# Performance work log

Hardware: AMD Instinct MI355X
Metric: run time of the kernel (lower is better)

The kernel has to match this reference:

```python
import jax, jax.numpy as jnp
import numpy as np

EPS = 1e-7  # tf.keras.backend.epsilon()


def squash(v, axis=-1):
    s = jnp.sum(jnp.square(v), axis=axis, keepdims=True)
    scale = s / (1.0 + s) / jnp.sqrt(s + EPS)
    return scale * v


def setup_inputs() -> dict:
    key = jax.random.key(0)
    k1, k2 = jax.random.split(key)
    B, I, D = 64, 2048, 16   # batch, input_num_capsule, input_dim_capsule
    J, K = 32, 16            # num_capsule, dim_capsule
    inputs = jax.random.normal(k1, (B, I, D), dtype=jnp.float32)
    # glorot_uniform-ish init for W: [in_caps, num_caps, in_dim, dim_caps]
    limit = np.sqrt(6.0 / (D + K)).astype(np.float32)
    W = jax.random.uniform(k2, (I, J, D, K), dtype=jnp.float32, minval=-limit, maxval=limit)
    return {"inputs": inputs, "W": W}


def reference(inputs, W, routings=3):
    # u_hat[b,i,j,:] = inputs[b,i,:] @ W[i,j,:,:]
    u_hat = jnp.einsum('bid,ijdk->bijk', inputs, W)  # [B, I, J, K]
    B, I, J, _ = u_hat.shape
    b = jnp.zeros((B, I, J, 1), dtype=u_hat.dtype)
    outputs = None
    for r in range(routings):
        c = jax.nn.softmax(b, axis=2)                              # [B, I, J, 1]
        outputs = squash(jnp.sum(c * u_hat, axis=1, keepdims=True))  # [B, 1, J, K]
        if r < routings - 1:
            b = b + jnp.sum(u_hat * outputs, axis=-1, keepdims=True)
    return jnp.squeeze(outputs, axis=1)  # [B, J, K]
```

## Files before the change

kernel.cpp:

```cpp
#include <hip/hip_runtime.h>
#include <hip/hip_bf16.h>


#define B_ 64
#define I_ 2048
#define D_ 16
#define J_ 32
#define K_ 16
#define JK 512

typedef __attribute__((ext_vector_type(8))) short short8;
typedef __attribute__((ext_vector_type(4))) float float4v;

__device__ __forceinline__ unsigned short f2bf(float f) {
    union { float f; unsigned int i; } v;
    v.f = f;
    const unsigned int x = v.i;
    return (unsigned short)((x + 0x7fffu + ((x >> 16) & 1u)) >> 16);
}

__device__ __forceinline__ void unpack8(const uint4 r, float* u) {
    union { unsigned int i; float f; } t;
    t.i = r.x << 16;         u[0] = t.f;
    t.i = r.x & 0xffff0000u; u[1] = t.f;
    t.i = r.y << 16;         u[2] = t.f;
    t.i = r.y & 0xffff0000u; u[3] = t.f;
    t.i = r.z << 16;         u[4] = t.f;
    t.i = r.z & 0xffff0000u; u[5] = t.f;
    t.i = r.w << 16;         u[6] = t.f;
    t.i = r.w & 0xffff0000u; u[7] = t.f;
}

template <int CTRL>
__device__ __forceinline__ float dpp_add(float x) {
    union { float f; int i; } a, b;
    a.f = x;
    b.i = __builtin_amdgcn_update_dpp(0, a.i, CTRL, 0xf, 0xf, false);
    return x + b.f;
}

__global__ __launch_bounds__(256)
void caps_produce(const float* __restrict__ x, const float* __restrict__ W,
                  unsigned short* __restrict__ uhat) {
    __shared__ unsigned short wlds[32 * 384];
    __shared__ unsigned short zbuf[8];
    const int i = blockIdx.x;
    const int tid = threadIdx.x;

    if (tid < 8) zbuf[tid] = 0;

    const int lane = tid & 63;
    const int wv = tid >> 6;
    const int quad = lane >> 4;
    const int l15 = lane & 15;
    const int b = wv * 16 + l15;

    union { uint4 u; short8 s; } bfrag;
    {
        const float* xp = x + ((size_t)b * I_ + i) * D_ + (quad & 1) * 8;
        const float4 x0 = reinterpret_cast<const float4*>(xp)[0];
        const float4 x1 = reinterpret_cast<const float4*>(xp)[1];
        bfrag.u.x = ((unsigned int)f2bf(x0.y) << 16) | f2bf(x0.x);
        bfrag.u.y = ((unsigned int)f2bf(x0.w) << 16) | f2bf(x0.z);
        bfrag.u.z = ((unsigned int)f2bf(x1.y) << 16) | f2bf(x1.x);
        bfrag.u.w = ((unsigned int)f2bf(x1.w) << 16) | f2bf(x1.z);
        if (quad >= 2) { bfrag.u.x = 0; bfrag.u.y = 0; bfrag.u.z = 0; bfrag.u.w = 0; }
    }

    {
        const float* wbase = W + (size_t)i * (J_ * D_ * K_);
        const int k = tid & 15;
#pragma unroll
        for (int half = 0; half < 2; ++half) {
            const int j = (tid >> 4) + half * 16;
            const float* p = wbase + j * (D_ * K_) + k;
            float vals[16];
#pragma unroll
            for (int d = 0; d < 16; ++d) vals[d] = p[d * K_];
            unsigned int pk[8];
#pragma unroll
            for (int q = 0; q < 8; ++q)
                pk[q] = ((unsigned int)f2bf(vals[2 * q + 1]) << 16) |
                        f2bf(vals[2 * q]);
            uint4* dst = reinterpret_cast<uint4*>(wlds + j * 384 + k * 24);
            uint4 w0; w0.x = pk[0]; w0.y = pk[1]; w0.z = pk[2]; w0.w = pk[3];
            uint4 w1; w1.x = pk[4]; w1.y = pk[5]; w1.z = pk[6]; w1.w = pk[7];
            dst[0] = w0; dst[1] = w1;
        }
    }
    __syncthreads();

    const unsigned short* aptr =
        (quad >= 2) ? zbuf : (wlds + l15 * 24 + (quad & 1) * 8);
    const int astride = (quad >= 2) ? 0 : 384;

    unsigned short* ub = uhat + ((size_t)i * B_ + b) * JK + quad * 4;

#pragma unroll
    for (int j = 0; j < 32; ++j) {
        union { uint4 u; short8 s; } af;
        af.u = *reinterpret_cast<const uint4*>(aptr + (size_t)j * astride);
        float4v acc = {0.f, 0.f, 0.f, 0.f};
        acc = __builtin_amdgcn_mfma_f32_16x16x32_bf16(af.s, bfrag.s, acc,
                                                      0, 0, 0);
        uint2 pk;
        pk.x = ((unsigned int)f2bf(acc[1]) << 16) | f2bf(acc[0]);
        pk.y = ((unsigned int)f2bf(acc[3]) << 16) | f2bf(acc[2]);
        *reinterpret_cast<uint2*>(ub + j * 16) = pk;
    }
}

__global__ __launch_bounds__(256)
void caps_sum0(const unsigned short* __restrict__ uhat,
               float* __restrict__ spart2) {
    __shared__ float part[4][512];
    const int bq = blockIdx.x;
    const int b = bq >> 5, q = bq & 31;
    const int lane = threadIdx.x & 63;
    const int w = threadIdx.x >> 6;

    const unsigned short* up =
        uhat + ((size_t)(q * 64 + w * 16) * B_ + b) * JK + lane * 8;
    const size_t istride = (size_t)B_ * JK;

    float acc[8];
#pragma unroll
    for (int k = 0; k < 8; ++k) acc[k] = 0.f;

    for (int ii = 0; ii < 16; ii += 4) {
        uint4 r[4];
#pragma unroll
        for (int s = 0; s < 4; ++s)
            r[s] = *reinterpret_cast<const uint4*>(up + (size_t)(ii + s) * istride);
#pragma unroll
        for (int s = 0; s < 4; ++s) {
            float u[8];
            unpack8(r[s], u);
#pragma unroll
            for (int k = 0; k < 8; ++k) acc[k] += u[k];
        }
    }

    float4 o0, o1;
    o0.x = acc[0]; o0.y = acc[1]; o0.z = acc[2]; o0.w = acc[3];
    o1.x = acc[4]; o1.y = acc[5]; o1.z = acc[6]; o1.w = acc[7];
    reinterpret_cast<float4*>(&part[w][lane * 8])[0] = o0;
    reinterpret_cast<float4*>(&part[w][lane * 8])[1] = o1;
    __syncthreads();

    const int t = threadIdx.x;
#pragma unroll
    for (int e = 0; e < 2; ++e) {
        const int jk = t * 2 + e;
        spart2[(size_t)bq * 512 + jk] =
            part[0][jk] + part[1][jk] + part[2][jk] + part[3][jk];
    }
}

__global__ __launch_bounds__(512)
void caps_squash0(const float* __restrict__ spart2, float* __restrict__ vsum) {
    const int bl = blockIdx.x;
    const int jk = threadIdx.x;
    float s = 0.f;
#pragma unroll
    for (int p = 0; p < 32; ++p)
        s += spart2[(size_t)(bl * 32 + p) * 512 + jk];
    s *= (1.f / 32.f);
    float q = s * s;
    q += __shfl_xor(q, 1, 64);
    q += __shfl_xor(q, 2, 64);
    q += __shfl_xor(q, 4, 64);
    q += __shfl_xor(q, 8, 64);
    const float scale = q / ((1.f + q) * sqrtf(q + 1e-7f));
    vsum[bl * JK + jk] = scale * s;
}

__global__ __launch_bounds__(128)
void caps_route1(const unsigned short* __restrict__ uhat,
                 const float* __restrict__ vsum, float* __restrict__ spart) {
    __shared__ float mrg[32][17];
    const int tid = threadIdx.x;
    const int lane = tid & 63;
    const int wv = tid >> 6;
    const int bl = blockIdx.x >> 6;
    const int chunk = blockIdx.x & 63;
    const int h = lane >> 5;
    const int j = lane & 31;

    float v[16];
    {
        const float4* vp =
            reinterpret_cast<const float4*>(vsum + bl * JK + j * 16);
        const float4 a0 = vp[0], a1 = vp[1], a2 = vp[2], a3 = vp[3];
        v[0] = a0.x; v[1] = a0.y; v[2] = a0.z; v[3] = a0.w;
        v[4] = a1.x; v[5] = a1.y; v[6] = a1.z; v[7] = a1.w;
        v[8] = a2.x; v[9] = a2.y; v[10] = a2.z; v[11] = a2.w;
        v[12] = a3.x; v[13] = a3.y; v[14] = a3.z; v[15] = a3.w;
    }

    float acc[16];
#pragma unroll
    for (int k = 0; k < 16; ++k) acc[k] = 0.f;

    const unsigned short* up =
        uhat + ((size_t)(chunk * 32 + wv * 16 + h) * B_ + bl) * JK + j * 16;
    const size_t istride2 = (size_t)2 * B_ * JK;

    uint4 c0 = reinterpret_cast<const uint4*>(up)[0];
    uint4 c1 = reinterpret_cast<const uint4*>(up)[1];

#pragma unroll 4
    for (int t = 0; t < 8; ++t) {
        uint4 n0, n1;
        if (t < 7) {
            const uint4* np =
                reinterpret_cast<const uint4*>(up + (size_t)(t + 1) * istride2);
            n0 = np[0];
            n1 = np[1];
        }
        float u[16];
        unpack8(c0, u);
        unpack8(c1, u + 8);
        float p = 0.f;
#pragma unroll
        for (int k = 0; k < 16; ++k) p += u[k] * v[k];
        const float e = __expf(p);
        float S = e;
        S = dpp_add<0x111>(S);
        S = dpp_add<0x112>(S);
        S = dpp_add<0x114>(S);
        S = dpp_add<0x118>(S);
        S = dpp_add<0x142>(S);
        union { float f; int i; } sv, lo, hi;
        sv.f = S;
        lo.i = __builtin_amdgcn_readlane(sv.i, 31);
        hi.i = __builtin_amdgcn_readlane(sv.i, 63);
        const float Ssel = (h == 0) ? lo.f : hi.f;
        const float c = e * __builtin_amdgcn_rcpf(Ssel);
#pragma unroll
        for (int k = 0; k < 16; ++k) acc[k] += c * u[k];
        c0 = n0;
        c1 = n1;
    }

#pragma unroll
    for (int k = 0; k < 16; ++k) acc[k] += __shfl_xor(acc[k], 32, 64);

    if (wv == 1 && h == 0) {
#pragma unroll
        for (int k = 0; k < 16; ++k) mrg[j][k] = acc[k];
    }
    __syncthreads();

    if (wv == 0 && h == 0) {
        float* sp = spart + ((size_t)chunk * B_ + bl) * JK + j * 16;
#pragma unroll
        for (int q = 0; q < 4; ++q) {
            float4 o;
            o.x = acc[q * 4 + 0] + mrg[j][q * 4 + 0];
            o.y = acc[q * 4 + 1] + mrg[j][q * 4 + 1];
            o.z = acc[q * 4 + 2] + mrg[j][q * 4 + 2];
            o.w = acc[q * 4 + 3] + mrg[j][q * 4 + 3];
            reinterpret_cast<float4*>(sp)[q] = o;
        }
    }
}

template <int MODE>
__global__ __launch_bounds__(512)
void caps_squash(const float* __restrict__ spart, float* __restrict__ vsum,
                 float* __restrict__ out) {
    const int bl = blockIdx.x;
    const int jk = threadIdx.x;
    float s = 0.f;
#pragma unroll 8
    for (int p = 0; p < 64; ++p)
        s += spart[((size_t)p * B_ + bl) * JK + jk];
    float q = s * s;
    q += __shfl_xor(q, 1, 64);
    q += __shfl_xor(q, 2, 64);
    q += __shfl_xor(q, 4, 64);
    q += __shfl_xor(q, 8, 64);
    const float scale = q / ((1.f + q) * sqrtf(q + 1e-7f));
    const float v = scale * s;
    if (MODE == 1) vsum[bl * JK + jk] += v;
    else           out[(size_t)bl * JK + jk] = v;
}

extern "C" void kernel_launch(void* const* d_in, const int* in_sizes, int n_in,
                              void* d_out, int out_size, void* d_ws,
                              size_t ws_size, hipStream_t stream) {
    const float* x = (const float*)d_in[0];
    const float* W = (const float*)d_in[1];
    float* out = (float*)d_out;

    char* ws = (char*)d_ws;
    unsigned short* uhat = (unsigned short*)ws;
    float* spart = (float*)(ws + (size_t)B_ * I_ * JK * 2);
    float* vsum = spart + (size_t)64 * B_ * JK;

    caps_produce<<<I_, 256, 0, stream>>>(x, W, uhat);

    caps_sum0<<<2048, 256, 0, stream>>>(uhat, spart);
    caps_squash0<<<B_, 512, 0, stream>>>(spart, vsum);

    caps_route1<<<4096, 128, 0, stream>>>(uhat, vsum, spart);
    caps_squash<1><<<B_, 512, 0, stream>>>(spart, vsum, out);

    caps_route1<<<4096, 128, 0, stream>>>(uhat, vsum, spart);
    caps_squash<2><<<B_, 512, 0, stream>>>(spart, vsum, out);
}
```

Baseline: 209.8 us.

## Recompute u_hat on the fly per routing pass instead of materializing it

Drops the materialized bf16 u_hat buffer and instead recomputes u_hat with MFMA in each routing pass, fusing the agreement dot product, softmax over capsules (via an LDS exchange between the two j-halves) and the weighted sum into one kernel. Each block handles eight input capsules with double-buffered W tiles in LDS and writes per-block partial sums that a squash kernel reduces. This removes the large u_hat write and the repeated re-reads of it, at the cost of re-reading W and x and repeating the matmul three times (twice per pass in routing mode). Only 256 blocks launch, which may underfill the GPU, and the squash reduction now walks 256 partials instead of 64.

New measurement: 229.9 us. 9.6% more time.

```diff
diff --git a/kernel.cpp b/kernel.cpp
--- a/kernel.cpp
+++ b/kernel.cpp
@@ -8,6 +8,8 @@
 #define J_ 32
 #define K_ 16
 #define JK 512
+#define NBLK 256
+#define GI 8
 
 typedef __attribute__((ext_vector_type(8))) short short8;
 typedef __attribute__((ext_vector_type(4))) float float4v;
@@ -19,61 +21,49 @@
     return (unsigned short)((x + 0x7fffu + ((x >> 16) & 1u)) >> 16);
 }
 
-__device__ __forceinline__ void unpack8(const uint4 r, float* u) {
-    union { unsigned int i; float f; } t;
-    t.i = r.x << 16;         u[0] = t.f;
-    t.i = r.x & 0xffff0000u; u[1] = t.f;
-    t.i = r.y << 16;         u[2] = t.f;
-    t.i = r.y & 0xffff0000u; u[3] = t.f;
-    t.i = r.z << 16;         u[4] = t.f;
-    t.i = r.z & 0xffff0000u; u[5] = t.f;
-    t.i = r.w << 16;         u[6] = t.f;
-    t.i = r.w & 0xffff0000u; u[7] = t.f;
-}
-
-template <int CTRL>
-__device__ __forceinline__ float dpp_add(float x) {
-    union { float f; int i; } a, b;
-    a.f = x;
-    b.i = __builtin_amdgcn_update_dpp(0, a.i, CTRL, 0xf, 0xf, false);
-    return x + b.f;
-}
-
-__global__ __launch_bounds__(256)
-void caps_produce(const float* __restrict__ x, const float* __restrict__ W,
-                  unsigned short* __restrict__ uhat) {
-    __shared__ unsigned short wlds[32 * 384];
+template <int MODE>
+__global__ __launch_bounds__(512)
+void caps_pass(const float* __restrict__ x, const float* __restrict__ W,
+               const float* __restrict__ vsum, float* __restrict__ part) {
+    __shared__ unsigned short wlds[2][32 * 384];
     __shared__ unsigned short zbuf[8];
-    const int i = blockIdx.x;
+    __shared__ float ebuf[2][4][2][16];
     const int tid = threadIdx.x;
+    const int lane = tid & 63;
+    const int wv = tid >> 6;
+    const int bt = wv & 3;
+    const int jh = wv >> 2;
+    const int quad = lane >> 4;
+    const int l15 = lane & 15;
+    const int b = bt * 16 + l15;
+    const int i0 = blockIdx.x * GI;
 
     if (tid < 8) zbuf[tid] = 0;
 
-    const int lane = tid & 63;
-    const int wv = tid >> 6;
-    const int quad = lane >> 4;
-    const int l15 = lane & 15;
-    const int b = wv * 16 + l15;
-
-    union { uint4 u; short8 s; } bfrag;
-    {
-        const float* xp = x + ((size_t)b * I_ + i) * D_ + (quad & 1) * 8;
-        const float4 x0 = reinterpret_cast<const float4*>(xp)[0];
-        const float4 x1 = reinterpret_cast<const float4*>(xp)[1];
-        bfrag.u.x = ((unsigned int)f2bf(x0.y) << 16) | f2bf(x0.x);
-        bfrag.u.y = ((unsigned int)f2bf(x0.w) << 16) | f2bf(x0.z);
-        bfrag.u.z = ((unsigned int)f2bf(x1.y) << 16) | f2bf(x1.x);
-        bfrag.u.w = ((unsigned int)f2bf(x1.w) << 16) | f2bf(x1.z);
-        if (quad >= 2) { bfrag.u.x = 0; bfrag.u.y = 0; bfrag.u.z = 0; bfrag.u.w = 0; }
+    float4 vv[16];
+    if (MODE == 1) {
+#pragma unroll
+        for (int jj = 0; jj < 16; ++jj)
+            vv[jj] = reinterpret_cast<const float4*>(
+                vsum + b * JK + (jh * 16 + jj) * 16 + quad * 4)[0];
     }
 
-    {
-        const float* wbase = W + (size_t)i * (J_ * D_ * K_);
-        const int k = tid & 15;
+    float4 acc2[16];
 #pragma unroll
-        for (int half = 0; half < 2; ++half) {
-            const int j = (tid >> 4) + half * 16;
-            const float* p = wbase + j * (D_ * K_) + k;
+    for (int jj = 0; jj < 16; ++jj) {
+        acc2[jj].x = 0.f; acc2[jj].y = 0.f;
+        acc2[jj].z = 0.f; acc2[jj].w = 0.f;
+    }
+
+    const int sk = tid & 15;
+    const int sj = tid >> 4;
+
+    for (int t = 0; t < GI; ++t) {
+        const int i = i0 + t;
+        const int par = t & 1;
+
+        {
+            const float* p = W + (size_t)i * (J_ * D_ * K_) + sj * (D_ * K_) + sk;
             float vals[16];
 #pragma unroll
             for (int d = 0; d < 16; ++d) vals[d] = p[d * K_];
@@ -82,200 +72,96 @@
             for (int q = 0; q < 8; ++q)
                 pk[q] = ((unsigned int)f2bf(vals[2 * q + 1]) << 16) |
                         f2bf(vals[2 * q]);
-            uint4* dst = reinterpret_cast<uint4*>(wlds + j * 384 + k * 24);
+            uint4* dst = reinterpret_cast<uint4*>(&wlds[par][sj * 384 + sk * 24]);
             uint4 w0; w0.x = pk[0]; w0.y = pk[1]; w0.z = pk[2]; w0.w = pk[3];
             uint4 w1; w1.x = pk[4]; w1.y = pk[5]; w1.z = pk[6]; w1.w = pk[7];
             dst[0] = w0; dst[1] = w1;
         }
-    }
-    __syncthreads();
 
-    const unsigned short* aptr =
-        (quad >= 2) ? zbuf : (wlds + l15 * 24 + (quad & 1) * 8);
-    const int astride = (quad >= 2) ? 0 : 384;
+        union { uint4 u; short8 s; } bfrag;
+        {
+            const float* xp = x + ((size_t)b * I_ + i) * D_ + (quad & 1) * 8;
+            const float4 x0 = reinterpret_cast<const float4*>(xp)[0];
+            const float4 x1 = reinterpret_cast<const float4*>(xp)[1];
+            bfrag.u.x = ((unsigned int)f2bf(x0.y) << 16) | f2bf(x0.x);
+            bfrag.u.y = ((unsigned int)f2bf(x0.w) << 16) | f2bf(x0.z);
+            bfrag.u.z = ((unsigned int)f2bf(x1.y) << 16) | f2bf(x1.x);
+            bfrag.u.w = ((unsigned int)f2bf(x1.w) << 16) | f2bf(x1.z);
+            if (quad >= 2) { bfrag.u.x = 0; bfrag.u.y = 0; bfrag.u.z = 0; bfrag.u.w = 0; }
+        }
+        __syncthreads();
 
-    unsigned short* ub = uhat + ((size_t)i * B_ + b) * JK + quad * 4;
+        const unsigned short* aptr =
+            (quad >= 2) ? zbuf : (&wlds[par][0] + l15 * 24 + (quad & 1) * 8);
+        const int astride = (quad >= 2) ? 0 : 384;
 
+        if (MODE == 0) {
 #pragma unroll
-    for (int j = 0; j < 32; ++j) {
-        union { uint4 u; short8 s; } af;
-        af.u = *reinterpret_cast<const uint4*>(aptr + (size_t)j * astride);
-        float4v acc = {0.f, 0.f, 0.f, 0.f};
-        acc = __builtin_amdgcn_mfma_f32_16x16x32_bf16(af.s, bfrag.s, acc,
-                                                      0, 0, 0);
-        uint2 pk;
-        pk.x = ((unsigned int)f2bf(acc[1]) << 16) | f2bf(acc[0]);
-        pk.y = ((unsigned int)f2bf(acc[3]) << 16) | f2bf(acc[2]);
-        *reinterpret_cast<uint2*>(ub + j * 16) = pk;
-    }
-}
-
-__global__ __launch_bounds__(256)
-void caps_sum0(const unsigned short* __restrict__ uhat,
-               float* __restrict__ spart2) {
-    __shared__ float part[4][512];
-    const int bq = blockIdx.x;
-    const int b = bq >> 5, q = bq & 31;
-    const int lane = threadIdx.x & 63;
-    const int w = threadIdx.x >> 6;
-
-    const unsigned short* up =
-        uhat + ((size_t)(q * 64 + w * 16) * B_ + b) * JK + lane * 8;
-    const size_t istride = (size_t)B_ * JK;
-
-    float acc[8];
+            for (int jj = 0; jj < 16; ++jj) {
+                const int j = jh * 16 + jj;
+                union { uint4 u; short8 s; } af;
+                af.u = *reinterpret_cast<const uint4*>(aptr + (size_t)j * astride);
+                float4v a = {0.f, 0.f, 0.f, 0.f};
+                a = __builtin_amdgcn_mfma_f32_16x16x32_bf16(af.s, bfrag.s, a,
+                                                            0, 0, 0);
+                acc2[jj].x += a[0]; acc2[jj].y += a[1];
+                acc2[jj].z += a[2]; acc2[jj].w += a[3];
+            }
+        } else {
+            float e[16];
+            float E = 0.f;
 #pragma unroll
-    for (int k = 0; k < 8; ++k) acc[k] = 0.f;
-
-    for (int ii = 0; ii < 16; ii += 4) {
-        uint4 r[4];
+            for (int jj = 0; jj < 16; ++jj) {
+                const int j = jh * 16 + jj;
+                union { uint4 u; short8 s; } af;
+                af.u = *reinterpret_cast<const uint4*>(aptr + (size_t)j * astride);
+                float4v a = {0.f, 0.f, 0.f, 0.f};
+                a = __builtin_amdgcn_mfma_f32_16x16x32_bf16(af.s, bfrag.s, a,
+                                                            0, 0, 0);
+                float p = a[0] * vv[jj].x + a[1] * vv[jj].y +
+                          a[2] * vv[jj].z + a[3] * vv[jj].w;
+                p += __shfl_xor(p, 16, 64);
+                p += __shfl_xor(p, 32, 64);
+                const float ee = __expf(p);
+                e[jj] = ee;
+                E += ee;
+            }
+            if (quad == 0) ebuf[par][bt][jh][l15] = E;
+            __syncthreads();
+            const float S = E + ebuf[par][bt][1 - jh][l15];
+            const float r = __builtin_amdgcn_rcpf(S);
 #pragma unroll
-        for (int s = 0; s < 4; ++s)
-            r[s] = *reinterpret_cast<const uint4*>(up + (size_t)(ii + s) * istride);
-#pragma unroll
-        for (int s = 0; s < 4; ++s) {
-            float u[8];
-            unpack8(r[s], u);
-#pragma unroll
-            for (int k = 0; k < 8; ++k) acc[k] += u[k];
+            for (int jj = 0; jj < 16; ++jj) {
+                const int j = jh * 16 + jj;
+                union { uint4 u; short8 s; } af;
+                af.u = *reinterpret_cast<const uint4*>(aptr + (size_t)j * astride);
+                float4v a = {0.f, 0.f, 0.f, 0.f};
+                a = __builtin_amdgcn_mfma_f32_16x16x32_bf16(af.s, bfrag.s, a,
+                                                            0, 0, 0);
+                const float c = e[jj] * r;
+                acc2[jj].x += c * a[0]; acc2[jj].y += c * a[1];
+                acc2[jj].z += c * a[2]; acc2[jj].w += c * a[3];
+            }
         }
     }
 
-    float4 o0, o1;
-    o0.x = acc[0]; o0.y = acc[1]; o0.z = acc[2]; o0.w = acc[3];
-    o1.x = acc[4]; o1.y = acc[5]; o1.z = acc[6]; o1.w = acc[7];
-    reinterpret_cast<float4*>(&part[w][lane * 8])[0] = o0;
-    reinterpret_cast<float4*>(&part[w][lane * 8])[1] = o1;
-    __syncthreads();
-
-    const int t = threadIdx.x;
+    float* pp = part + ((size_t)blockIdx.x * B_ + b) * JK + jh * 256 + quad * 4;
 #pragma unroll
-    for (int e = 0; e < 2; ++e) {
-        const int jk = t * 2 + e;
-        spart2[(size_t)bq * 512 + jk] =
-            part[0][jk] + part[1][jk] + part[2][jk] + part[3][jk];
-    }
-}
-
-__global__ __launch_bounds__(512)
-void caps_squash0(const float* __restrict__ spart2, float* __restrict__ vsum) {
-    const int bl = blockIdx.x;
-    const int jk = threadIdx.x;
-    float s = 0.f;
-#pragma unroll
-    for (int p = 0; p < 32; ++p)
-        s += spart2[(size_t)(bl * 32 + p) * 512 + jk];
-    s *= (1.f / 32.f);
-    float q = s * s;
-    q += __shfl_xor(q, 1, 64);
-    q += __shfl_xor(q, 2, 64);
-    q += __shfl_xor(q, 4, 64);
-    q += __shfl_xor(q, 8, 64);
-    const float scale = q / ((1.f + q) * sqrtf(q + 1e-7f));
-    vsum[bl * JK + jk] = scale * s;
-}
-
-__global__ __launch_bounds__(128)
-void caps_route1(const unsigned short* __restrict__ uhat,
-                 const float* __restrict__ vsum, float* __restrict__ spart) {
-    __shared__ float mrg[32][17];
-    const int tid = threadIdx.x;
-    const int lane = tid & 63;
-    const int wv = tid >> 6;
-    const int bl = blockIdx.x >> 6;
-    const int chunk = blockIdx.x & 63;
-    const int h = lane >> 5;
-    const int j = lane & 31;
-
-    float v[16];
-    {
-        const float4* vp =
-            reinterpret_cast<const float4*>(vsum + bl * JK + j * 16);
-        const float4 a0 = vp[0], a1 = vp[1], a2 = vp[2], a3 = vp[3];
-        v[0] = a0.x; v[1] = a0.y; v[2] = a0.z; v[3] = a0.w;
-        v[4] = a1.x; v[5] = a1.y; v[6] = a1.z; v[7] = a1.w;
-        v[8] = a2.x; v[9] = a2.y; v[10] = a2.z; v[11] = a2.w;
-        v[12] = a3.x; v[13] = a3.y; v[14] = a3.z; v[15] = a3.w;
-    }
-
-    float acc[16];
-#pragma unroll
-    for (int k = 0; k < 16; ++k) acc[k] = 0.f;
-
-    const unsigned short* up =
-        uhat + ((size_t)(chunk * 32 + wv * 16 + h) * B_ + bl) * JK + j * 16;
-    const size_t istride2 = (size_t)2 * B_ * JK;
-
-    uint4 c0 = reinterpret_cast<const uint4*>(up)[0];
-    uint4 c1 = reinterpret_cast<const uint4*>(up)[1];
-
-#pragma unroll 4
-    for (int t = 0; t < 8; ++t) {
-        uint4 n0, n1;
-        if (t < 7) {
-            const uint4* np =
-                reinterpret_cast<const uint4*>(up + (size_t)(t + 1) * istride2);
-            n0 = np[0];
-            n1 = np[1];
-        }
-        float u[16];
-        unpack8(c0, u);
-        unpack8(c1, u + 8);
-        float p = 0.f;
-#pragma unroll
-        for (int k = 0; k < 16; ++k) p += u[k] * v[k];
-        const float e = __expf(p);
-        float S = e;
-        S = dpp_add<0x111>(S);
-        S = dpp_add<0x112>(S);
-        S = dpp_add<0x114>(S);
-        S = dpp_add<0x118>(S);
-        S = dpp_add<0x142>(S);
-        union { float f; int i; } sv, lo, hi;
-        sv.f = S;
-        lo.i = __builtin_amdgcn_readlane(sv.i, 31);
-        hi.i = __builtin_amdgcn_readlane(sv.i, 63);
-        const float Ssel = (h == 0) ? lo.f : hi.f;
-        const float c = e * __builtin_amdgcn_rcpf(Ssel);
-#pragma unroll
-        for (int k = 0; k < 16; ++k) acc[k] += c * u[k];
-        c0 = n0;
-        c1 = n1;
-    }
-
-#pragma unroll
-    for (int k = 0; k < 16; ++k) acc[k] += __shfl_xor(acc[k], 32, 64);
-
-    if (wv == 1 && h == 0) {
-#pragma unroll
-        for (int k = 0; k < 16; ++k) mrg[j][k] = acc[k];
-    }
-    __syncthreads();
-
-    if (wv == 0 && h == 0) {
-        float* sp = spart + ((size_t)chunk * B_ + bl) * JK + j * 16;
-#pragma unroll
-        for (int q = 0; q < 4; ++q) {
-            float4 o;
-            o.x = acc[q * 4 + 0] + mrg[j][q * 4 + 0];
-            o.y = acc[q * 4 + 1] + mrg[j][q * 4 + 1];
-            o.z = acc[q * 4 + 2] + mrg[j][q * 4 + 2];
-            o.w = acc[q * 4 + 3] + mrg[j][q * 4 + 3];
-            reinterpret_cast<float4*>(sp)[q] = o;
-        }
-    }
+    for (int jj = 0; jj < 16; ++jj)
+        reinterpret_cast<float4*>(pp + jj * 16)[0] = acc2[jj];
 }
 
 template <int MODE>
 __global__ __launch_bounds__(512)
-void caps_squash(const float* __restrict__ spart, float* __restrict__ vsum,
-                 float* __restrict__ out) {
+void caps_squashN(const float* __restrict__ part, float* __restrict__ vsum,
+                  float* __restrict__ out) {
     const int bl = blockIdx.x;
     const int jk = threadIdx.x;
     float s = 0.f;
 #pragma unroll 8
-    for (int p = 0; p < 64; ++p)
-        s += spart[((size_t)p * B_ + bl) * JK + jk];
+    for (int p = 0; p < NBLK; ++p)
+        s += part[((size_t)p * B_ + bl) * JK + jk];
+    if (MODE == 0) s *= (1.f / 32.f);
     float q = s * s;
     q += __shfl_xor(q, 1, 64);
     q += __shfl_xor(q, 2, 64);
@@ -283,8 +169,9 @@
     q += __shfl_xor(q, 8, 64);
     const float scale = q / ((1.f + q) * sqrtf(q + 1e-7f));
     const float v = scale * s;
-    if (MODE == 1) vsum[bl * JK + jk] += v;
-    else           out[(size_t)bl * JK + jk] = v;
+    if (MODE == 0)      vsum[bl * JK + jk] = v;
+    else if (MODE == 1) vsum[bl * JK + jk] += v;
+    else                out[(size_t)bl * JK + jk] = v;
 }
 
 extern "C" void kernel_launch(void* const* d_in, const int* in_sizes, int n_in,
@@ -295,18 +182,14 @@
     float* out = (float*)d_out;
 
     char* ws = (char*)d_ws;
-    unsigned short* uhat = (unsigned short*)ws;
-    float* spart = (float*)(ws + (size_t)B_ * I_ * JK * 2);
-    float* vsum = spart + (size_t)64 * B_ * JK;
+    float* part = (float*)ws;
+    float* vsum =
+        (float*)(ws + (size_t)B_ * I_ * JK * 2 + (size_t)64 * B_ * JK * 4);
 
-    caps_produce<<<I_, 256, 0, stream>>>(x, W, uhat);
-
-    caps_sum0<<<2048, 256, 0, stream>>>(uhat, spart);
-    caps_squash0<<<B_, 512, 0, stream>>>(spart, vsum);
-
-    caps_route1<<<4096, 128, 0, stream>>>(uhat, vsum, spart);
-    caps_squash<1><<<B_, 512, 0, stream>>>(spart, vsum, out);
-
-    caps_route1<<<4096, 128, 0, stream>>>(uhat, vsum, spart);
-    caps_squash<2><<<B_, 512, 0, stream>>>(spart, vsum, out);
+    caps_pass<0><<<NBLK, 512, 0, stream>>>(x, W, nullptr, part);
+    caps_squashN<0><<<B_, 512, 0, stream>>>(part, vsum, nullptr);
+    caps_pass<1><<<NBLK, 512, 0, stream>>>(x, W, vsum, part);
+    caps_squashN<1><<<B_, 512, 0, stream>>>(part, vsum, nullptr);
+    caps_pass<1><<<NBLK, 512, 0, stream>>>(x, W, vsum, part);
+    caps_squashN<2><<<B_, 512, 0, stream>>>(part, vsum, out);
 }
```
